# Kernel optimization log

Measured on AMD Instinct MI355X. Metric: run time of the kernel, lower is better.

The kernel has to match this reference:

```python
import jax, jax.numpy as jnp
import numpy as np

# Dimensions (see shape_source)
IN_VEC = 131072          # input_vector_size
NUM_CAPS = 512           # num_capsules (output capsules)
CAP_SIZE = 256           # capsule_size
RF_SIZE = 64             # receptive_field_size
RF_PER_CAP = CAP_SIZE // RF_SIZE        # 4
IN_CAPS = IN_VEC // CAP_SIZE            # 512 input_eff_capsules
CONN_P = 0.1             # connection_probability


def setup_inputs() -> dict:
    key = jax.random.key(0)
    kx, kc, kw = jax.random.split(key, 3)
    x = jax.random.normal(kx, (IN_VEC,), dtype=jnp.float32)
    # Sparse ScRRAMBLe routing tensor: mostly zeros, gated by connection probability.
    # Shape (input_eff_capsules, rf_per_cap_in, num_capsules, rf_per_cap_out) per einsum 'ijkl,ijm->klm'.
    Ci = (jax.random.uniform(kc, (IN_CAPS, RF_PER_CAP, NUM_CAPS, RF_PER_CAP)) < CONN_P).astype(jnp.float32)
    # glorot_normal over last two axes: fan_in = fan_out = RF_SIZE -> std = sqrt(2/(64+64)) = 0.125
    glorot_std = float(np.sqrt(2.0 / (RF_SIZE + RF_SIZE)))
    Wi = glorot_std * jax.random.normal(kw, (NUM_CAPS, RF_PER_CAP, RF_PER_CAP, RF_SIZE, RF_SIZE), dtype=jnp.float32)
    return {"x": x, "Ci": Ci, "Wi": Wi}


def reference(x, Ci, Wi):
    # x: (IN_VEC,) -> (input_eff_capsules, rf_per_cap, rf_size)
    x_reshaped = x.reshape(IN_CAPS, RF_PER_CAP, RF_SIZE)
    # Route input receptive fields to output capsule slots:
    # x_routed: (num_capsules, rf_per_cap, rf_size)
    x_routed = jnp.einsum('ijkl,ijm->klm', Ci, x_reshaped)
    # Per-capsule small batched transform:
    # y: (num_capsules, rf_per_cap, rf_size)
    y = jnp.einsum('ijklm,ikm->ijl', Wi, x_routed)
    return y
```

## Files before the change

### kernel.cpp

```cpp
#include <hip/hip_runtime.h>


__global__ __launch_bounds__(256) void caps_fused(
    const float* __restrict__ x,
    const float* __restrict__ Ci,
    const float* __restrict__ Wi,
    float* __restrict__ y)
{
    const int i    = blockIdx.x;
    const int t    = threadIdx.x;
    const int lane = t & 63;

    __shared__ float part[16 * 256];
    __shared__ float xr[256];

    const int g   = t >> 4;
    const int mq4 = t & 15;

    const float4* __restrict__ Ci4 = reinterpret_cast<const float4*>(Ci);
    const float4* __restrict__ x4p = reinterpret_cast<const float4*>(x);

    float4 acc0 = make_float4(0.f, 0.f, 0.f, 0.f);
    float4 acc1 = make_float4(0.f, 0.f, 0.f, 0.f);
    float4 acc2 = make_float4(0.f, 0.f, 0.f, 0.f);
    float4 acc3 = make_float4(0.f, 0.f, 0.f, 0.f);

    const int ijbase = g << 7;
    #pragma unroll 4
    for (int it = 0; it < 128; ++it) {
        const int ij = ijbase + it;
        const float4 c4 = Ci4[ij * 512 + i];
        const float4 xv = x4p[(ij << 4) + mq4];
        acc0.x += c4.x * xv.x; acc0.y += c4.x * xv.y; acc0.z += c4.x * xv.z; acc0.w += c4.x * xv.w;
        acc1.x += c4.y * xv.x; acc1.y += c4.y * xv.y; acc1.z += c4.y * xv.z; acc1.w += c4.y * xv.w;
        acc2.x += c4.z * xv.x; acc2.y += c4.z * xv.y; acc2.z += c4.z * xv.z; acc2.w += c4.z * xv.w;
        acc3.x += c4.w * xv.x; acc3.y += c4.w * xv.y; acc3.z += c4.w * xv.z; acc3.w += c4.w * xv.w;
    }

    {
        float4* p4 = reinterpret_cast<float4*>(part);
        p4[(g << 6) + (0 << 4) + mq4] = acc0;
        p4[(g << 6) + (1 << 4) + mq4] = acc1;
        p4[(g << 6) + (2 << 4) + mq4] = acc2;
        p4[(g << 6) + (3 << 4) + mq4] = acc3;
    }
    __syncthreads();

    {
        float s = 0.f;
        #pragma unroll
        for (int gg = 0; gg < 16; ++gg) s += part[(gg << 8) + t];
        xr[t] = s;
    }
    __syncthreads();

    const int j   = t >> 6;
    const int lq  = lane >> 4;
    const int m16 = lane & 15;

    const float4* __restrict__ W4 = reinterpret_cast<const float4*>(Wi);
    const int wbase = (i * 4 + j) * 4096;

    float4 xr0 = reinterpret_cast<const float4*>(xr)[0 * 16 + m16];
    float4 xr1 = reinterpret_cast<const float4*>(xr)[1 * 16 + m16];
    float4 xr2 = reinterpret_cast<const float4*>(xr)[2 * 16 + m16];
    float4 xr3 = reinterpret_cast<const float4*>(xr)[3 * 16 + m16];

    #pragma unroll 4
    for (int l0 = 0; l0 < 64; l0 += 4) {
        const int l = l0 + lq;
        float p = 0.f;
        {
            const float4 w = W4[wbase + 0 * 1024 + l * 16 + m16];
            p += w.x * xr0.x + w.y * xr0.y + w.z * xr0.z + w.w * xr0.w;
        }
        {
            const float4 w = W4[wbase + 1 * 1024 + l * 16 + m16];
            p += w.x * xr1.x + w.y * xr1.y + w.z * xr1.z + w.w * xr1.w;
        }
        {
            const float4 w = W4[wbase + 2 * 1024 + l * 16 + m16];
            p += w.x * xr2.x + w.y * xr2.y + w.z * xr2.z + w.w * xr2.w;
        }
        {
            const float4 w = W4[wbase + 3 * 1024 + l * 16 + m16];
            p += w.x * xr3.x + w.y * xr3.y + w.z * xr3.z + w.w * xr3.w;
        }
        p += __shfl_xor(p, 1);
        p += __shfl_xor(p, 2);
        p += __shfl_xor(p, 4);
        p += __shfl_xor(p, 8);
        if (m16 == 0) y[(i * 4 + j) * 64 + l] = p;
    }
}

extern "C" void kernel_launch(void* const* d_in, const int* in_sizes, int n_in,
                              void* d_out, int out_size, void* d_ws, size_t ws_size,
                              hipStream_t stream) {
    const float* x  = (const float*)d_in[0];
    const float* Ci = (const float*)d_in[1];
    const float* Wi = (const float*)d_in[2];
    float* y = (float*)d_out;
    caps_fused<<<512, 256, 0, stream>>>(x, Ci, Wi, y);
}
```

Baseline: 232.7 us.

## Split fused capsule kernel into chunked routing and per-row transform kernels

The single fused kernel becomes two launches. The first splits the routing reduction over input capsules into up to four chunks (a 512x4 grid) and writes partial routed vectors to workspace. The second kernel, on 2048 blocks, sums those partials and does the Wi transform, with each block handling one (capsule, rf) slice. This gives more parallelism to hide the latency of the strided Ci and Wi loads. The cost is an extra launch, partial-sum traffic through global memory, and x being reloaded by more blocks.

```diff
diff --git a/kernel.cpp b/kernel.cpp
--- a/kernel.cpp
+++ b/kernel.cpp
@@ -1,33 +1,32 @@
 #include <hip/hip_runtime.h>
 
 
-__global__ __launch_bounds__(256) void caps_fused(
+__global__ __launch_bounds__(256) void route_kernel(
     const float* __restrict__ x,
     const float* __restrict__ Ci,
-    const float* __restrict__ Wi,
-    float* __restrict__ y)
+    float* __restrict__ xr_part,
+    int ijpc)
 {
-    const int i    = blockIdx.x;
-    const int t    = threadIdx.x;
-    const int lane = t & 63;
+    const int i = blockIdx.x;
+    const int c = blockIdx.y;
+    const int t = threadIdx.x;
+    const int g   = t >> 4;
+    const int mq4 = t & 15;
 
     __shared__ float part[16 * 256];
-    __shared__ float xr[256];
-
-    const int g   = t >> 4;
-    const int mq4 = t & 15;
 
     const float4* __restrict__ Ci4 = reinterpret_cast<const float4*>(Ci);
     const float4* __restrict__ x4p = reinterpret_cast<const float4*>(x);
 
-    float4 acc0 = make_float4(0.f, 0.f, 0.f, 0.f);
-    float4 acc1 = make_float4(0.f, 0.f, 0.f, 0.f);
-    float4 acc2 = make_float4(0.f, 0.f, 0.f, 0.f);
-    float4 acc3 = make_float4(0.f, 0.f, 0.f, 0.f);
+    float4 acc0 = make_float4(0.f,0.f,0.f,0.f);
+    float4 acc1 = make_float4(0.f,0.f,0.f,0.f);
+    float4 acc2 = make_float4(0.f,0.f,0.f,0.f);
+    float4 acc3 = make_float4(0.f,0.f,0.f,0.f);
 
-    const int ijbase = g << 7;
+    const int iters  = ijpc >> 4;
+    const int ijbase = c * ijpc + g * iters;
     #pragma unroll 4
-    for (int it = 0; it < 128; ++it) {
+    for (int it = 0; it < iters; ++it) {
         const int ij = ijbase + it;
         const float4 c4 = Ci4[ij * 512 + i];
         const float4 xv = x4p[(ij << 4) + mq4];
@@ -46,51 +45,69 @@
     }
     __syncthreads();
 
-    {
-        float s = 0.f;
-        #pragma unroll
-        for (int gg = 0; gg < 16; ++gg) s += part[(gg << 8) + t];
-        xr[t] = s;
+    float s = 0.f;
+    #pragma unroll
+    for (int gg = 0; gg < 16; ++gg) s += part[(gg << 8) + t];
+    xr_part[(c * 512 + i) * 256 + t] = s;
+}
+
+__global__ __launch_bounds__(256) void transform_kernel(
+    const float* __restrict__ Wi,
+    const float* __restrict__ xr_part,
+    float* __restrict__ y,
+    int nchunks)
+{
+    const int b    = blockIdx.x;
+    const int i    = b >> 2;
+    const int t    = threadIdx.x;
+    const int lane = t & 63;
+    const int w    = t >> 6;
+    const int lq   = lane >> 4;
+    const int m16  = lane & 15;
+
+    const float4* __restrict__ xp4 = reinterpret_cast<const float4*>(xr_part);
+    float4 xr0 = make_float4(0.f,0.f,0.f,0.f);
+    float4 xr1 = make_float4(0.f,0.f,0.f,0.f);
+    float4 xr2 = make_float4(0.f,0.f,0.f,0.f);
+    float4 xr3 = make_float4(0.f,0.f,0.f,0.f);
+    for (int c = 0; c < nchunks; ++c) {
+        const int base = (c * 512 + i) * 64;
+        float4 v;
+        v = xp4[base + 0*16 + m16]; xr0.x += v.x; xr0.y += v.y; xr0.z += v.z; xr0.w += v.w;
+        v = xp4[base + 1*16 + m16]; xr1.x += v.x; xr1.y += v.y; xr1.z += v.z; xr1.w += v.w;
+        v = xp4[base + 2*16 + m16]; xr2.x += v.x; xr2.y += v.y; xr2.z += v.z; xr2.w += v.w;
+        v = xp4[base + 3*16 + m16]; xr3.x += v.x; xr3.y += v.y; xr3.z += v.z; xr3.w += v.w;
     }
-    __syncthreads();
-
-    const int j   = t >> 6;
-    const int lq  = lane >> 4;
-    const int m16 = lane & 15;
 
     const float4* __restrict__ W4 = reinterpret_cast<const float4*>(Wi);
-    const int wbase = (i * 4 + j) * 4096;
+    const int wbase = b * 4096;
+    const int lw    = w << 4;
 
-    float4 xr0 = reinterpret_cast<const float4*>(xr)[0 * 16 + m16];
-    float4 xr1 = reinterpret_cast<const float4*>(xr)[1 * 16 + m16];
-    float4 xr2 = reinterpret_cast<const float4*>(xr)[2 * 16 + m16];
-    float4 xr3 = reinterpret_cast<const float4*>(xr)[3 * 16 + m16];
-
-    #pragma unroll 4
-    for (int l0 = 0; l0 < 64; l0 += 4) {
-        const int l = l0 + lq;
+    #pragma unroll
+    for (int c2 = 0; c2 < 4; ++c2) {
+        const int l = lw + (c2 << 2) + lq;
         float p = 0.f;
         {
-            const float4 w = W4[wbase + 0 * 1024 + l * 16 + m16];
-            p += w.x * xr0.x + w.y * xr0.y + w.z * xr0.z + w.w * xr0.w;
+            const float4 wv = W4[wbase + 0*1024 + l*16 + m16];
+            p += wv.x*xr0.x + wv.y*xr0.y + wv.z*xr0.z + wv.w*xr0.w;
         }
         {
-            const float4 w = W4[wbase + 1 * 1024 + l * 16 + m16];
-            p += w.x * xr1.x + w.y * xr1.y + w.z * xr1.z + w.w * xr1.w;
+            const float4 wv = W4[wbase + 1*1024 + l*16 + m16];
+            p += wv.x*xr1.x + wv.y*xr1.y + wv.z*xr1.z + wv.w*xr1.w;
         }
         {
-            const float4 w = W4[wbase + 2 * 1024 + l * 16 + m16];
-            p += w.x * xr2.x + w.y * xr2.y + w.z * xr2.z + w.w * xr2.w;
+            const float4 wv = W4[wbase + 2*1024 + l*16 + m16];
+            p += wv.x*xr2.x + wv.y*xr2.y + wv.z*xr2.z + wv.w*xr2.w;
         }
         {
-            const float4 w = W4[wbase + 3 * 1024 + l * 16 + m16];
-            p += w.x * xr3.x + w.y * xr3.y + w.z * xr3.z + w.w * xr3.w;
+            const float4 wv = W4[wbase + 3*1024 + l*16 + m16];
+            p += wv.x*xr3.x + wv.y*xr3.y + wv.z*xr3.z + wv.w*xr3.w;
         }
         p += __shfl_xor(p, 1);
         p += __shfl_xor(p, 2);
         p += __shfl_xor(p, 4);
         p += __shfl_xor(p, 8);
-        if (m16 == 0) y[(i * 4 + j) * 64 + l] = p;
+        if (m16 == 0) y[b * 64 + l] = p;
     }
 }
 
@@ -100,6 +117,12 @@
     const float* x  = (const float*)d_in[0];
     const float* Ci = (const float*)d_in[1];
     const float* Wi = (const float*)d_in[2];
-    float* y = (float*)d_out;
-    caps_fused<<<512, 256, 0, stream>>>(x, Ci, Wi, y);
+    float* y  = (float*)d_out;
+    float* xr = (float*)d_ws;
+
+    int nchunks = (ws_size >= (size_t)4 * 512 * 256 * sizeof(float)) ? 4 : 1;
+    int ijpc    = 2048 / nchunks;
+
+    route_kernel<<<dim3(512, nchunks), 256, 0, stream>>>(x, Ci, xr, ijpc);
+    transform_kernel<<<2048, 256, 0, stream>>>(Wi, xr, y, nchunks);
 }
```

Measured after the change: 231.4 us. About the same (-0.6%).
